# Kernel optimization log

Measured on AMD Instinct MI355X. Metric: run time of the kernel, lower is better.

## Reference

```python
import jax, jax.numpy as jnp
import numpy as np
import math

CROP_H, CROP_W = 384, 512
MAX_FLOW = (CROP_H * CROP_W) ** 0.5
VAR_MAX, VAR_MIN = 10.0, 0.0
LOG2 = math.log(2.0)
N_PRED, B = 12, 4


def setup_inputs() -> dict:
    key = jax.random.key(0)
    k1, k2, k3 = jax.random.split(key, 3)
    flow_preds = jax.random.normal(k1, (N_PRED, B, 2, CROP_H, CROP_W), dtype=jnp.float32)
    info_preds = jax.random.normal(k2, (N_PRED, B, 4, CROP_H, CROP_W), dtype=jnp.float32)
    flow_gt = jax.random.normal(k3, (B, 2, CROP_H, CROP_W), dtype=jnp.float32)
    valid = jnp.ones((B, 1, CROP_H, CROP_W), dtype=jnp.float32)
    auxiliary = jnp.ones((1,), dtype=jnp.float32)
    return {"flow_preds": flow_preds, "info_preds": info_preds,
            "flow_gt": flow_gt, "valid": valid, "auxiliary": auxiliary}


def reference(flow_preds, info_preds, flow_gt, valid, auxiliary):
    # mask from flow magnitude and validity (detached in original)
    mag = jnp.sqrt(jnp.sum(flow_gt ** 2, axis=1, keepdims=True))  # [B,1,H,W]
    mask1 = (mag < MAX_FLOW) & (valid != 0)                       # [B,1,H,W]
    mask2 = jnp.broadcast_to(mask1, flow_gt.shape)                # [B,2,H,W]

    def step_loss(flow, info):
        # flow: [B,2,H,W], info: [B,4,H,W]
        alpha = info[:, :2]                                       # mixture logits [B,2,H,W]
        log_b = jnp.stack([
            jnp.clip(info[:, 2], 0.0, VAR_MAX),
            jnp.clip(info[:, 3], VAR_MIN, 0.0),                   # clamps to exactly 0 (as in source)
        ], axis=1)                                                # [B,2,H,W]
        # term2: [B, flow_ch=2, comp=2, H, W]
        term2 = jnp.abs(flow_gt - flow)[:, :, None] * jnp.exp(-log_b)[:, None]
        term1 = alpha - LOG2 - log_b                              # [B,2,H,W]
        nf = (jax.nn.logsumexp(alpha, axis=1, keepdims=True)
              - jax.nn.logsumexp(term1[:, None] - term2, axis=2))  # [B,2,H,W]
        fm = jnp.isfinite(jax.lax.stop_gradient(nf)) & mask2
        cnt = jnp.maximum(jnp.sum(fm).astype(nf.dtype), 1.0)
        return jnp.sum(jnp.where(fm, nf, 0.0)) / cnt

    lap_losses = jax.vmap(step_loss)(flow_preds, info_preds)      # [N_PRED]
    lap_loss = jnp.sum(lap_losses)

    degenerate = jnp.mean(mask1.astype(jnp.float32)) < 0.25
    zero_path = 0.0 * (jnp.mean(flow_preds) + jnp.mean(info_preds))
    loss = jnp.where(degenerate, zero_path, lap_loss)

    loss = loss + 0.0 * jnp.sum(auxiliary)
    return loss
```

## Files before the change

### kernel.cpp

```cpp
#include <hip/hip_runtime.h>
#include <math.h>

#define Hc 384
#define Wc 512
#define Bc 4
#define NP 12
#define HWc (Hc * Wc)
#define Pc (Bc * HWc)
#define MAX_FLOW_C 443.40500673763256f
#define LOG2_C 0.69314718055994530942f
#define L2E_C  1.44269504088896340736f

#define NCH 2
#define NSPC 6
#define NBG 768
#define NQ 25

typedef float vf4 __attribute__((ext_vector_type(4)));

__device__ __forceinline__ float fexp2(float x) {
#if __has_builtin(__builtin_amdgcn_exp2f)
    return __builtin_amdgcn_exp2f(x);
#else
    return exp2f(x);
#endif
}
__device__ __forceinline__ float flog2(float x) {
#if __has_builtin(__builtin_amdgcn_logf)
    return __builtin_amdgcn_logf(x);
#else
    return log2f(x);
#endif
}

__device__ __forceinline__ float lse22(float a, float b) {
    float m = fmaxf(a, b);
    float d = fminf(a, b) - m;
    return m + flog2(1.0f + fexp2(d));
}

__device__ __forceinline__ vf4 ldnt4(const float* p) {
    return __builtin_nontemporal_load((const vf4*)p);
}

__global__ __launch_bounds__(256) void loss_part(
    const float* __restrict__ fp,
    const float* __restrict__ ip,
    const float* __restrict__ gt,
    const float* __restrict__ valid,
    float* __restrict__ part) {

    const int chunk = blockIdx.x & (NCH - 1);
    const int gb    = blockIdx.x >> 1;
    const int g  = gb * 256 + threadIdx.x;
    const int b  = g / (HWc / 4);
    const int hw = (g % (HWc / 4)) * 4;
    const int n0 = chunk * NSPC;

    const vf4 gx4 = *(const vf4*)(gt + ((size_t)b * 2 + 0) * HWc + hw);
    const vf4 gy4 = *(const vf4*)(gt + ((size_t)b * 2 + 1) * HWc + hw);
    const vf4 vv4 = *(const vf4*)(valid + (size_t)b * HWc + hw);

    float gxa[4] = {gx4.x, gx4.y, gx4.z, gx4.w};
    float gya[4] = {gy4.x, gy4.y, gy4.z, gy4.w};
    float vva[4] = {vv4.x, vv4.y, vv4.z, vv4.w};

    bool  m1[4];
    float mcnt = 0.0f;
#pragma unroll
    for (int j = 0; j < 4; ++j) {
        float mag = sqrtf(gxa[j] * gxa[j] + gya[j] * gya[j]);
        m1[j] = (mag < MAX_FLOW_C) && (vva[j] != 0.0f);
        mcnt += m1[j] ? 1.0f : 0.0f;
    }

    float s[NSPC];
    float c[NSPC];
#pragma unroll
    for (int k = 0; k < NSPC; ++k) { s[k] = 0.0f; c[k] = 0.0f; }

#pragma unroll
    for (int k = 0; k < NSPC; ++k) {
        const int n = n0 + k;
        const float* fbase = fp + ((size_t)(n * Bc + b) * 2) * HWc + hw;
        const float* ibase = ip + ((size_t)(n * Bc + b) * 4) * HWc + hw;

        const vf4 fx4 = ldnt4(fbase);
        const vf4 fy4 = ldnt4(fbase + HWc);
        const vf4 a04 = ldnt4(ibase);
        const vf4 a14 = ldnt4(ibase + HWc);
        const vf4 lb4 = ldnt4(ibase + 2 * (size_t)HWc);

        float fxa[4] = {fx4.x, fx4.y, fx4.z, fx4.w};
        float fya[4] = {fy4.x, fy4.y, fy4.z, fy4.w};
        float a0a[4] = {a04.x, a04.y, a04.z, a04.w};
        float a1a[4] = {a14.x, a14.y, a14.z, a14.w};
        float lba[4] = {lb4.x, lb4.y, lb4.z, lb4.w};

#pragma unroll
        for (int j = 0; j < 4; ++j) {
            float LB  = fminf(fmaxf(lba[j], 0.0f), 10.0f) * L2E_C;
            float e2  = fexp2(-LB);
            float A0  = a0a[j] * L2E_C;
            float A1  = a1a[j] * L2E_C;
            float lsa = lse22(A0, A1);
            float t10 = A0 - 1.0f - LB;
            float t11 = A1 - 1.0f;
            float D0  = fabsf(gxa[j] - fxa[j]) * L2E_C;
            float D1  = fabsf(gya[j] - fya[j]) * L2E_C;

            float nf0 = lsa - lse22(t10 - D0 * e2, t11 - D0);
            float nf1 = lsa - lse22(t10 - D1 * e2, t11 - D1);

            bool ok0 = m1[j] && isfinite(nf0);
            bool ok1 = m1[j] && isfinite(nf1);
            s[k] += ok0 ? nf0 : 0.0f;
            c[k] += ok0 ? 1.0f : 0.0f;
            s[k] += ok1 ? nf1 : 0.0f;
            c[k] += ok1 ? 1.0f : 0.0f;
        }
    }

#pragma unroll
    for (int k = 0; k < NSPC; ++k) {
        for (int off = 32; off > 0; off >>= 1) {
            s[k] += __shfl_down(s[k], off);
            c[k] += __shfl_down(c[k], off);
        }
    }
    for (int off = 32; off > 0; off >>= 1) mcnt += __shfl_down(mcnt, off);

    __shared__ float red[4][2 * NSPC + 1];
    const int lane = threadIdx.x & 63;
    const int wid  = threadIdx.x >> 6;
    if (lane == 0) {
#pragma unroll
        for (int k = 0; k < NSPC; ++k) {
            red[wid][k]        = s[k];
            red[wid][NSPC + k] = c[k];
        }
        red[wid][2 * NSPC] = mcnt;
    }
    __syncthreads();
    if (threadIdx.x < 2 * NSPC + 1) {
        float v = red[0][threadIdx.x] + red[1][threadIdx.x] +
                  red[2][threadIdx.x] + red[3][threadIdx.x];
        int q;
        if (threadIdx.x < NSPC)           q = n0 + threadIdx.x;
        else if (threadIdx.x < 2 * NSPC)  q = 12 + n0 + threadIdx.x - NSPC;
        else                              q = 24;
        if (q != 24 || chunk == 0)
            part[(size_t)q * NBG + gb] = v;
    }
}

__global__ __launch_bounds__(256) void loss_reduce(
    const float* __restrict__ part, float* __restrict__ acc2) {
    const int q = blockIdx.x;
    const float* p = part + (size_t)q * NBG;
    float v = 0.0f;
    for (int i = threadIdx.x; i < NBG; i += 256) v += p[i];
    for (int off = 32; off > 0; off >>= 1) v += __shfl_down(v, off);
    __shared__ float r[4];
    if ((threadIdx.x & 63) == 0) r[threadIdx.x >> 6] = v;
    __syncthreads();
    if (threadIdx.x == 0) acc2[q] = r[0] + r[1] + r[2] + r[3];
}

__global__ void loss_final(const float* __restrict__ acc2, float* __restrict__ out) {
    if (blockIdx.x == 0 && threadIdx.x == 0) {
        float loss = 0.0f;
#pragma unroll
        for (int n = 0; n < NP; ++n)
            loss += LOG2_C * acc2[n] / fmaxf(acc2[12 + n], 1.0f);
        float mean_mask = acc2[24] / (float)Pc;
        out[0] = (mean_mask < 0.25f) ? 0.0f : loss;
    }
}

extern "C" void kernel_launch(void* const* d_in, const int* in_sizes, int n_in,
                              void* d_out, int out_size, void* d_ws, size_t ws_size,
                              hipStream_t stream) {
    const float* fp    = (const float*)d_in[0];
    const float* ip    = (const float*)d_in[1];
    const float* gt    = (const float*)d_in[2];
    const float* valid = (const float*)d_in[3];
    float* part = (float*)d_ws;
    float* acc2 = part + (size_t)NQ * NBG;

    loss_part<<<NBG * NCH, 256, 0, stream>>>(fp, ip, gt, valid, part);
    loss_reduce<<<NQ, 256, 0, stream>>>(part, acc2);
    loss_final<<<1, 64, 0, stream>>>(acc2, (float*)d_out);
}
```

Measured before the change: 250.5 us.

## Split predictions into three chunks and fuse reduce and final kernels

Changes the work split from 2 chunks of 6 predictions to 3 chunks of 4, using a 2D grid, and adds an occupancy hint to the launch bounds. This yields more blocks with fewer registers each. The two tail kernels (per-quantity reduce and final combine) are merged into a single 512-thread block, removing one launch and the intermediate buffer. The trade-off is that gt/valid loads are repeated across three chunks instead of two.

```diff
diff --git a/kernel.cpp b/kernel.cpp
--- a/kernel.cpp
+++ b/kernel.cpp
@@ -11,8 +11,8 @@
 #define LOG2_C 0.69314718055994530942f
 #define L2E_C  1.44269504088896340736f
 
-#define NCH 2
-#define NSPC 6
+#define NCH 3
+#define NSPC 4
 #define NBG 768
 #define NQ 25
 
@@ -43,15 +43,15 @@
     return __builtin_nontemporal_load((const vf4*)p);
 }
 
-__global__ __launch_bounds__(256) void loss_part(
+__global__ __launch_bounds__(256, 4) void loss_part(
     const float* __restrict__ fp,
     const float* __restrict__ ip,
     const float* __restrict__ gt,
     const float* __restrict__ valid,
     float* __restrict__ part) {
 
-    const int chunk = blockIdx.x & (NCH - 1);
-    const int gb    = blockIdx.x >> 1;
+    const int chunk = blockIdx.y;
+    const int gb    = blockIdx.x;
     const int g  = gb * 256 + threadIdx.x;
     const int b  = g / (HWc / 4);
     const int hw = (g % (HWc / 4)) * 4;
@@ -154,26 +154,25 @@
     }
 }
 
-__global__ __launch_bounds__(256) void loss_reduce(
-    const float* __restrict__ part, float* __restrict__ acc2) {
-    const int q = blockIdx.x;
-    const float* p = part + (size_t)q * NBG;
-    float v = 0.0f;
-    for (int i = threadIdx.x; i < NBG; i += 256) v += p[i];
-    for (int off = 32; off > 0; off >>= 1) v += __shfl_down(v, off);
-    __shared__ float r[4];
-    if ((threadIdx.x & 63) == 0) r[threadIdx.x >> 6] = v;
+__global__ __launch_bounds__(512) void loss_tail(
+    const float* __restrict__ part, float* __restrict__ out) {
+    __shared__ float sq[NQ];
+    const int lane = threadIdx.x & 63;
+    const int wid  = threadIdx.x >> 6;
+    for (int q = wid; q < NQ; q += 8) {
+        const float* p = part + (size_t)q * NBG;
+        float v = 0.0f;
+        for (int i = lane; i < NBG; i += 64) v += p[i];
+        for (int off = 32; off > 0; off >>= 1) v += __shfl_down(v, off);
+        if (lane == 0) sq[q] = v;
+    }
     __syncthreads();
-    if (threadIdx.x == 0) acc2[q] = r[0] + r[1] + r[2] + r[3];
-}
-
-__global__ void loss_final(const float* __restrict__ acc2, float* __restrict__ out) {
-    if (blockIdx.x == 0 && threadIdx.x == 0) {
+    if (threadIdx.x == 0) {
         float loss = 0.0f;
 #pragma unroll
         for (int n = 0; n < NP; ++n)
-            loss += LOG2_C * acc2[n] / fmaxf(acc2[12 + n], 1.0f);
-        float mean_mask = acc2[24] / (float)Pc;
+            loss += LOG2_C * sq[n] / fmaxf(sq[12 + n], 1.0f);
+        float mean_mask = sq[24] / (float)Pc;
         out[0] = (mean_mask < 0.25f) ? 0.0f : loss;
     }
 }
@@ -186,9 +185,7 @@
     const float* gt    = (const float*)d_in[2];
     const float* valid = (const float*)d_in[3];
     float* part = (float*)d_ws;
-    float* acc2 = part + (size_t)NQ * NBG;
 
-    loss_part<<<NBG * NCH, 256, 0, stream>>>(fp, ip, gt, valid, part);
-    loss_reduce<<<NQ, 256, 0, stream>>>(part, acc2);
-    loss_final<<<1, 64, 0, stream>>>(acc2, (float*)d_out);
+    loss_part<<<dim3(NBG, NCH), 256, 0, stream>>>(fp, ip, gt, valid, part);
+    loss_tail<<<1, 512, 0, stream>>>(part, (float*)d_out);
 }
```

After: 264.2 us. +5.5%, slower.
